# Kernel tuning notes

Measured on AMD Instinct MI355X. Metric: run time of the kernel, lower is better.

The kernel has to match this reference:

```python
import jax, jax.numpy as jnp
import numpy as np

ROPE_BASE = 10000.0

def _rope(x):
    # x: (B, T, H, hd); rotate-half RoPE
    B, T, H, hd = x.shape
    half = hd // 2
    inv_freq = 1.0 / (ROPE_BASE ** (jnp.arange(half, dtype=jnp.float32) / half))
    ang = jnp.arange(T, dtype=jnp.float32)[:, None] * inv_freq[None, :]  # (T, half)
    cos = jnp.cos(ang)[None, :, None, :]
    sin = jnp.sin(ang)[None, :, None, :]
    x1, x2 = x[..., :half], x[..., half:]
    return jnp.concatenate([x1 * cos - x2 * sin, x1 * sin + x2 * cos], axis=-1)

def setup_inputs() -> dict:
    key = jax.random.key(0)
    k1, k2, k3 = jax.random.split(key, 3)
    B, T, D = 4, 2048, 2048
    x = jax.random.normal(k1, (B, T, D), dtype=jnp.float32)
    attn_mask = jnp.ones((B, T), dtype=bool)
    w_qkv = jax.random.normal(k2, (3 * D, D), dtype=jnp.float32) * (D ** -0.5)
    w_out = jax.random.normal(k3, (D, D), dtype=jnp.float32) * (D ** -0.5)
    return {"x": x, "attn_mask": attn_mask, "is_causal": 1, "w_qkv": w_qkv, "w_out": w_out}

def reference(x, attn_mask, is_causal, w_qkv, w_out):
    B, T, D = x.shape
    H = 16
    hd = D // H
    qkv = jnp.einsum('btd,ed->bte', x, w_qkv)  # (B, T, 3D)
    q, k, v = jnp.split(qkv, 3, axis=2)
    q = _rope(q.reshape(B, T, H, hd))
    k = _rope(k.reshape(B, T, H, hd))
    v = v.reshape(B, T, H, hd)
    scale = 1.0 / jnp.sqrt(jnp.float32(hd))
    scores = jnp.einsum('bqhd,bkhd->bhqk', q, k) * scale  # (B, H, T, T)
    if is_causal:
        mask = jnp.tril(jnp.ones((T, T), dtype=bool))[None, None]
    else:
        mask = attn_mask[:, None, None, :]  # (B,1,1,T)
    scores = jnp.where(mask, scores, jnp.finfo(scores.dtype).min)
    attn = jax.nn.softmax(scores, axis=-1)
    y = jnp.einsum('bhqk,bkhd->bqhd', attn, v).reshape(B, T, D)
    return jnp.einsum('btd,ed->bte', y, w_out)
```

## Files before the change

kernel.cpp:

```cpp
#include <hip/hip_runtime.h>
#include <stdint.h>
#include <stddef.h>

typedef float f32x4 __attribute__((ext_vector_type(4)));
typedef __bf16 bf16x8 __attribute__((ext_vector_type(8)));
typedef short s16x4 __attribute__((ext_vector_type(4)));

#define DEVI static __device__ __forceinline__

DEVI float bf2f(unsigned short u) {
  unsigned int x = ((unsigned int)u) << 16;
  float f;
  __builtin_memcpy(&f, &x, 4);
  return f;
}
DEVI unsigned short f2bf(float f) {
  unsigned int x;
  __builtin_memcpy(&x, &f, 4);
  unsigned int r = (x + 0x7fffu + ((x >> 16) & 1u)) >> 16;
  return (unsigned short)r;
}

DEVI void async16(const void* g, void* l) {
  __builtin_amdgcn_global_load_lds((__attribute__((address_space(1))) void*)g,
                                   (__attribute__((address_space(3))) void*)l,
                                   16, 0, 0);
}

#define BAR_LGKM()                                          \
  do {                                                      \
    asm volatile("s_waitcnt lgkmcnt(0)" ::: "memory");      \
    __builtin_amdgcn_s_barrier();                           \
    __builtin_amdgcn_sched_barrier(0);                      \
  } while (0)

#define BAR_VM(N)                                               \
  do {                                                          \
    asm volatile("s_waitcnt vmcnt(" #N ")" ::: "memory");       \
    __builtin_amdgcn_s_barrier();                               \
    __builtin_amdgcn_sched_barrier(0);                          \
  } while (0)

__global__ __launch_bounds__(256) void cvt_bf16(const float* __restrict__ in,
                                                unsigned short* __restrict__ out, int n) {
  int i = (blockIdx.x * 256 + threadIdx.x) * 4;
  if (i >= n) return;
  float4 v = *(const float4*)(in + i);
  s16x4 o;
  o[0] = (short)f2bf(v.x);
  o[1] = (short)f2bf(v.y);
  o[2] = (short)f2bf(v.z);
  o[3] = (short)f2bf(v.w);
  *(s16x4*)(out + i) = o;
}

__global__ __launch_bounds__(256) void rope_table(float* __restrict__ tab) {
  int idx = blockIdx.x * 256 + threadIdx.x;
  if (idx >= 2048 * 64) return;
  int tt = idx >> 6, j = idx & 63;
  float inv = powf(10000.0f, -(float)j * (1.0f / 64.0f));
  float ang = (float)tt * inv;
  tab[tt * 128 + j] = cosf(ang);
  tab[tt * 128 + 64 + j] = sinf(ang);
}

__global__ __launch_bounds__(256) void rope_apply(unsigned short* __restrict__ Qg,
                                                  unsigned short* __restrict__ Kg,
                                                  const float* __restrict__ tab) {
  const float S2 = 0.0883883476483184f * 1.44269504088896341f;
  int idx = blockIdx.x * 256 + threadIdx.x;
  int j4 = idx & 15;
  int tt = (idx >> 4) & 2047;
  int bh = idx >> 15;
  size_t base = ((size_t)bh * 2048 + tt) * 128;
  f32x4 c4 = *(const f32x4*)(tab + tt * 128 + j4 * 4);
  f32x4 s4 = *(const f32x4*)(tab + tt * 128 + 64 + j4 * 4);
  s16x4 q1 = *(const s16x4*)(Qg + base + j4 * 4);
  s16x4 q2 = *(const s16x4*)(Qg + base + 64 + j4 * 4);
  s16x4 k1 = *(const s16x4*)(Kg + base + j4 * 4);
  s16x4 k2 = *(const s16x4*)(Kg + base + 64 + j4 * 4);
  s16x4 o1, o2, p1, p2;
#pragma unroll
  for (int r = 0; r < 4; ++r) {
    float c = c4[r], s = s4[r];
    float a = bf2f((unsigned short)q1[r]), b2 = bf2f((unsigned short)q2[r]);
    o1[r] = (short)f2bf((a * c - b2 * s) * S2);
    o2[r] = (short)f2bf((a * s + b2 * c) * S2);
    float ka = bf2f((unsigned short)k1[r]), kb = bf2f((unsigned short)k2[r]);
    p1[r] = (short)f2bf(ka * c - kb * s);
    p2[r] = (short)f2bf(ka * s + kb * c);
  }
  *(s16x4*)(Qg + base + j4 * 4) = o1;
  *(s16x4*)(Qg + base + 64 + j4 * 4) = o2;
  *(s16x4*)(Kg + base + j4 * 4) = p1;
  *(s16x4*)(Kg + base + 64 + j4 * 4) = p2;
}

template <int EPI>
__global__ __launch_bounds__(512) void gemm256(const unsigned short* __restrict__ A,
                                               const unsigned short* __restrict__ B,
                                               float* __restrict__ C, int M, int N, int K,
                                               unsigned short* __restrict__ Q,
                                               unsigned short* __restrict__ Kk,
                                               unsigned short* __restrict__ VT) {
  __shared__ __attribute__((aligned(128))) unsigned short Al[2][2][8192];
  __shared__ __attribute__((aligned(128))) unsigned short Bl[2][2][8192];
  const int t = threadIdx.x;
  const int lane = t & 63;
  const int w = t >> 6, wr = w >> 2, wc = w & 3;
  const int g = lane >> 4, lr = lane & 15;

  const int id = blockIdx.y * gridDim.x + blockIdx.x;
  const int nwg = gridDim.x * gridDim.y;
  const int wg = (id & 7) * (nwg >> 3) + (id >> 3);
  const int bm = (wg / gridDim.x) * 256, bn = (wg % gridDim.x) * 256;

  const unsigned short* aptr = A + (size_t)bm * K;
  const unsigned short* bptr = B + (size_t)bn * K;

  const int srow = t >> 3;
  const int sslot = (t & 7) ^ (srow & 7);

#define STG(arr, mat, p, h, kt)                                                   \
  do {                                                                            \
    const unsigned short* _s =                                                    \
        (mat) + (size_t)((h) * 128 + srow) * K + (size_t)(kt) * 64 + sslot * 8;   \
    async16(_s, &arr[p][h][t * 8]);                                               \
    async16(_s + (size_t)64 * K, &arr[p][h][t * 8 + 4096]);                       \
  } while (0)

  const int u0 = ((g ^ (lr & 7)) * 8) + lr * 64;
  const int u1 = (((4 + g) ^ (lr & 7)) * 8) + lr * 64;

#define LDA(p, mh)                                                                \
  _Pragma("unroll") for (int mf = 0; mf < 4; ++mf) {                              \
    af[mf][0] = *(const bf16x8*)&Al[p][wr][(mh) * 4096 + mf * 1024 + u0];         \
    af[mf][1] = *(const bf16x8*)&Al[p][wr][(mh) * 4096 + mf * 1024 + u1];         \
  }
#define LDB(p, nh)                                                                \
  _Pragma("unroll") for (int nf = 0; nf < 2; ++nf) {                              \
    bfr[nf][0] = *(const bf16x8*)&Bl[p][wc >> 1][(wc & 1) * 4096 + (nh) * 2048 +  \
                                                 nf * 1024 + u0];                 \
    bfr[nf][1] = *(const bf16x8*)&Bl[p][wc >> 1][(wc & 1) * 4096 + (nh) * 2048 +  \
                                                 nf * 1024 + u1];                 \
  }
#define MMA(mh, nh)                                                               \
  __builtin_amdgcn_s_setprio(1);                                                  \
  _Pragma("unroll") for (int mf = 0; mf < 4; ++mf)                                \
      _Pragma("unroll") for (int nf = 0; nf < 2; ++nf) {                          \
    acc[(mh) * 4 + mf][(nh) * 2 + nf] = __builtin_amdgcn_mfma_f32_16x16x32_bf16(  \
        af[mf][0], bfr[nf][0], acc[(mh) * 4 + mf][(nh) * 2 + nf], 0, 0, 0);       \
    acc[(mh) * 4 + mf][(nh) * 2 + nf] = __builtin_amdgcn_mfma_f32_16x16x32_bf16(  \
        af[mf][1], bfr[nf][1], acc[(mh) * 4 + mf][(nh) * 2 + nf], 0, 0, 0);       \
  }                                                                               \
  __builtin_amdgcn_s_setprio(0);
#define PH_PRE()                                           \
  do {                                                     \
    __builtin_amdgcn_s_barrier();                          \
    asm volatile("s_waitcnt lgkmcnt(0)" ::: "memory");     \
    __builtin_amdgcn_sched_barrier(0);                     \
  } while (0)
#define PH_POST() __builtin_amdgcn_s_barrier();

  f32x4 acc[8][4] = {};

  STG(Al, aptr, 0, 0, 0);
  STG(Al, aptr, 0, 1, 0);
  STG(Bl, bptr, 0, 0, 0);
  STG(Bl, bptr, 0, 1, 0);
  STG(Bl, bptr, 1, 0, 1);
  STG(Bl, bptr, 1, 1, 1);
  asm volatile("s_waitcnt vmcnt(4)" ::: "memory");
  __builtin_amdgcn_s_barrier();
  __builtin_amdgcn_sched_barrier(0);

  const int NITER = K >> 7;
  for (int i = 0; i < NITER; ++i) {
    const bool G = (i + 1 < NITER);
    const int t1 = 2 * i + 1, t2 = 2 * i + 2, t3 = 2 * i + 3;
    bf16x8 af[4][2], bfr[2][2];

    LDA(0, 0);
    LDB(0, 0);
    STG(Al, aptr, 1, 0, t1);
    STG(Al, aptr, 1, 1, t1);
    PH_PRE();
    MMA(0, 0);
    PH_POST();
    LDA(0, 1);
    PH_PRE();
    MMA(1, 0);
    PH_POST();
    LDB(0, 1);
    PH_PRE();
    MMA(1, 1);
    PH_POST();
    LDA(0, 0);
    if (G) {
      STG(Bl, bptr, 0, 0, t2);
      asm volatile("s_waitcnt vmcnt(2)" ::: "memory");
    } else {
      asm volatile("s_waitcnt vmcnt(0)" ::: "memory");
    }
    PH_PRE();
    MMA(0, 1);
    PH_POST();
    LDA(1, 0);
    LDB(1, 0);
    if (G) STG(Bl, bptr, 0, 1, t2);
    PH_PRE();
    MMA(0, 0);
    PH_POST();
    LDA(1, 1);
    if (G) STG(Al, aptr, 0, 0, t2);
    PH_PRE();
    MMA(1, 0);
    PH_POST();
    LDB(1, 1);
    if (G) STG(Al, aptr, 0, 1, t2);
    PH_PRE();
    MMA(1, 1);
    PH_POST();
    LDA(1, 0);
    if (G) {
      STG(Bl, bptr, 1, 0, t3);
      STG(Bl, bptr, 1, 1, t3);
      asm volatile("s_waitcnt vmcnt(4)" ::: "memory");
    }
    PH_PRE();
    MMA(0, 1);
    PH_POST();
  }
#undef STG
#undef LDA
#undef LDB
#undef MMA
#undef PH_PRE
#undef PH_POST

  if (EPI == 0) {
#pragma unroll
    for (int mp = 0; mp < 8; ++mp) {
      int m0 = bm + wr * 128 + (mp >> 2) * 64 + (mp & 3) * 16 + g * 4;
#pragma unroll
      for (int nfi = 0; nfi < 4; ++nfi) {
        int n = bn + wc * 64 + (nfi >> 1) * 32 + (nfi & 1) * 16 + lr;
#pragma unroll
        for (int r = 0; r < 4; ++r) C[(size_t)(m0 + r) * N + n] = acc[mp][nfi][r];
      }
    }
  } else {
    const int bi = bm >> 11;
    const int tbase = bm & 2047;
#pragma unroll
    for (int nfi = 0; nfi < 4; ++nfi) {
      int e = bn + wc * 64 + (nfi >> 1) * 32 + (nfi & 1) * 16 + lr;
      int region = e >> 11;
      int e2 = e & 2047;
      int h = e2 >> 7, d = e2 & 127;
      int bh = bi * 16 + h;
#pragma unroll
      for (int mp = 0; mp < 8; ++mp) {
        int trow = tbase + wr * 128 + (mp >> 2) * 64 + (mp & 3) * 16 + g * 4;
        if (region == 2) {
          s16x4 pk;
#pragma unroll
          for (int r = 0; r < 4; ++r) pk[r] = (short)f2bf(acc[mp][nfi][r]);
          *(s16x4*)(VT + ((size_t)bh * 128 + d) * 2048 + trow) = pk;
        } else {
          unsigned short* dst = (region == 0) ? Q : Kk;
#pragma unroll
          for (int r = 0; r < 4; ++r)
            dst[((size_t)bh * 2048 + trow + r) * 128 + d] = f2bf(acc[mp][nfi][r]);
        }
      }
    }
  }
}

__global__ __launch_bounds__(256) void flash_attn(const unsigned short* __restrict__ Qg,
                                                  const unsigned short* __restrict__ Kg,
                                                  const unsigned short* __restrict__ VTg,
                                                  unsigned short* __restrict__ Yg,
                                                  const int* __restrict__ iscausal,
                                                  const unsigned char* __restrict__ amask) {
  __shared__ __attribute__((aligned(128))) unsigned short Ks[2][64 * 128];
  __shared__ __attribute__((aligned(128))) unsigned short Vs[2][128 * 64];
  __shared__ __attribute__((aligned(128))) unsigned short Ps[4][16 * 72];

  const int t = threadIdx.x, lane = t & 63, w = t >> 6;
  const int g = lane >> 4, lr = lane & 15;
  const int id = blockIdx.x;
  const int xcd = id & 7, j5 = id >> 3;
  const int bh = xcd * 8 + (j5 >> 5);
  const int qbi = 31 - (j5 & 31);
  const int b = bh >> 4;
  const int qb = qbi * 64;
  const int causal = iscausal[0] != 0;
  const int nt = causal ? (qbi + 1) : 32;

  const unsigned short* qrow = Qg + ((size_t)bh * 2048 + qb + w * 16 + lr) * 128;
  bf16x8 qf[4];
#pragma unroll
  for (int ds = 0; ds < 4; ++ds) qf[ds] = *(const bf16x8*)(qrow + ds * 32 + g * 8);

  const unsigned short* Kbase = Kg + (size_t)bh * 2048 * 128;
  const unsigned short* Vbase = VTg + (size_t)bh * 128 * 2048;

  const int rK = t >> 4, sK = ((t & 15) ^ rK);
  const int rV = t >> 3, sV = ((t & 7) ^ ((t >> 3) & 7));

#define STAGE(KT, P)                                                                    \
  do {                                                                                  \
    const int _kv = (KT) * 64;                                                          \
    _Pragma("unroll") for (int c = 0; c < 4; ++c)                                       \
        async16(Kbase + (size_t)(_kv + c * 16 + rK) * 128 + sK * 8,                     \
                &Ks[P][c * 2048 + t * 8]);                                              \
    _Pragma("unroll") for (int c = 0; c < 4; ++c)                                       \
        async16(Vbase + (size_t)(c * 32 + rV) * 2048 + _kv + sV * 8,                    \
                &Vs[P][c * 2048 + t * 8]);                                              \
  } while (0)

  unsigned int oi[4] = {0x3F803F80u, 0x3F803F80u, 0x3F803F80u, 0x3F803F80u};
  bf16x8 ones;
  __builtin_memcpy(&ones, oi, 16);

  f32x4 acc[8] = {};
  f32x4 accl = {0.f, 0.f, 0.f, 0.f};
  float mrow[4] = {-1e30f, -1e30f, -1e30f, -1e30f};

  STAGE(0, 0);

  for (int kt = 0; kt < nt; ++kt) {
    const int p = kt & 1;
    const int kv0 = kt * 64;
    if (kt + 1 < nt) {
      STAGE(kt + 1, p ^ 1);
      BAR_VM(8);
    } else {
      BAR_VM(0);
    }

    f32x4 s[4] = {};
    __builtin_amdgcn_s_setprio(1);
#pragma unroll
    for (int cf = 0; cf < 4; ++cf)
#pragma unroll
      for (int ds = 0; ds < 4; ++ds) {
        bf16x8 kf = *(const bf16x8*)(&Ks[p][(cf * 16 + lr) * 128 + (((ds * 4 + g) ^ lr) * 8)]);
        s[cf] = __builtin_amdgcn_mfma_f32_16x16x32_bf16(qf[ds], kf, s[cf], 0, 0, 0);
      }
    __builtin_amdgcn_s_setprio(0);

    const int q0 = qb + w * 16 + g * 4;
    if (causal) {
      if (kt == qbi) {
#pragma unroll
        for (int cf = 0; cf < 4; ++cf) {
          int kvg = kv0 + cf * 16 + lr;
#pragma unroll
          for (int r = 0; r < 4; ++r)
            if (kvg > q0 + r) s[cf][r] = -1e30f;
        }
      }
    } else {
#pragma unroll
      for (int cf = 0; cf < 4; ++cf) {
        int kvg = kv0 + cf * 16 + lr;
        if (!amask[(size_t)b * 2048 + kvg]) {
#pragma unroll
          for (int r = 0; r < 4; ++r) s[cf][r] = -1e30f;
        }
      }
    }

    f32x4 lm;
#pragma unroll
    for (int r = 0; r < 4; ++r)
      lm[r] = fmaxf(fmaxf(s[0][r], s[1][r]), fmaxf(s[2][r], s[3][r]));
    bool ok = true;
#pragma unroll
    for (int r = 0; r < 4; ++r) ok = ok && (lm[r] <= mrow[r] + 8.0f);
    if (!__all(ok)) {
      f32x4 mx = lm;
#pragma unroll
      for (int off = 8; off >= 1; off >>= 1)
#pragma unroll
        for (int r = 0; r < 4; ++r) mx[r] = fmaxf(mx[r], __shfl_xor(mx[r], off));
#pragma unroll
      for (int r = 0; r < 4; ++r) {
        float mn = fmaxf(mrow[r], mx[r]);
        float corr = exp2f(mrow[r] - mn);
        mrow[r] = mn;
        accl[r] *= corr;
#pragma unroll
        for (int jf = 0; jf < 8; ++jf) acc[jf][r] *= corr;
      }
    }

#pragma unroll
    for (int cf = 0; cf < 4; ++cf)
#pragma unroll
      for (int r = 0; r < 4; ++r) s[cf][r] = exp2f(s[cf][r] - mrow[r]);

    unsigned short* Pw = &Ps[w][0];
#pragma unroll
    for (int cf = 0; cf < 4; ++cf)
#pragma unroll
      for (int r = 0; r < 4; ++r) Pw[(g * 4 + r) * 72 + cf * 16 + lr] = f2bf(s[cf][r]);
    asm volatile("s_waitcnt lgkmcnt(0)" ::: "memory");
    __builtin_amdgcn_sched_barrier(0);

    bf16x8 pa0 = *(const bf16x8*)(Pw + lr * 72 + g * 8);
    bf16x8 pa1 = *(const bf16x8*)(Pw + lr * 72 + 32 + g * 8);

    accl = __builtin_amdgcn_mfma_f32_16x16x32_bf16(pa0, ones, accl, 0, 0, 0);
    accl = __builtin_amdgcn_mfma_f32_16x16x32_bf16(pa1, ones, accl, 0, 0, 0);

    __builtin_amdgcn_s_setprio(1);
#pragma unroll
    for (int jf = 0; jf < 8; ++jf) {
      bf16x8 v0 = *(const bf16x8*)(&Vs[p][(jf * 16 + lr) * 64 + ((g ^ (lr & 7)) * 8)]);
      bf16x8 v1 = *(const bf16x8*)(&Vs[p][(jf * 16 + lr) * 64 + (((4 + g) ^ (lr & 7)) * 8)]);
      acc[jf] = __builtin_amdgcn_mfma_f32_16x16x32_bf16(pa0, v0, acc[jf], 0, 0, 0);
      acc[jf] = __builtin_amdgcn_mfma_f32_16x16x32_bf16(pa1, v1, acc[jf], 0, 0, 0);
    }
    __builtin_amdgcn_s_setprio(0);

    BAR_LGKM();
  }
#undef STAGE

  const int h = bh & 15;
  float rl[4];
#pragma unroll
  for (int r = 0; r < 4; ++r) rl[r] = __builtin_amdgcn_rcpf(accl[r]);
#pragma unroll
  for (int jf = 0; jf < 8; ++jf)
#pragma unroll
    for (int r = 0; r < 4; ++r) {
      int tt = qb + w * 16 + g * 4 + r;
      Yg[((size_t)b * 2048 + tt) * 2048 + h * 128 + jf * 16 + lr] = f2bf(acc[jf][r] * rl[r]);
    }
}

extern "C" void kernel_launch(void* const* d_in, const int* in_sizes, int n_in, void* d_out,
                              int out_size, void* d_ws, size_t ws_size, hipStream_t stream) {
  const float* x = (const float*)d_in[0];
  const unsigned char* amask = (const unsigned char*)d_in[1];
  const int* iscausal = (const int*)d_in[2];
  const float* wqkv = (const float*)d_in[3];
  const float* wout = (const float*)d_in[4];
  float* out = (float*)d_out;

  const size_t MT = 8192, D = 2048, ND = 6144;
  unsigned short* xb = (unsigned short*)d_ws;
  unsigned short* wqkvb = xb + MT * D;
  unsigned short* woutb = wqkvb + ND * D;
  unsigned short* q = woutb + D * D;
  unsigned short* k = q + MT * D;
  unsigned short* vt = k + MT * D;
  unsigned short* y = vt + MT * D;
  float* tab = (float*)(y + MT * D);
  if (ws_size < (size_t)(100663296) * 2 + 2048 * 128 * 4) return;

  cvt_bf16<<<dim3(16384), dim3(256), 0, stream>>>(x, xb, (int)(MT * D));
  cvt_bf16<<<dim3(12288), dim3(256), 0, stream>>>(wqkv, wqkvb, (int)(ND * D));
  cvt_bf16<<<dim3(4096), dim3(256), 0, stream>>>(wout, woutb, (int)(D * D));
  rope_table<<<dim3(512), dim3(256), 0, stream>>>(tab);
  gemm256<1><<<dim3(24, 32), dim3(512), 0, stream>>>(xb, wqkvb, nullptr, 8192, 6144, 2048, q, k, vt);
  rope_apply<<<dim3(8192), dim3(256), 0, stream>>>(q, k, tab);
  flash_attn<<<dim3(2048), dim3(256), 0, stream>>>(q, k, vt, y, iscausal, amask);
  gemm256<0><<<dim3(8, 32), dim3(512), 0, stream>>>(y, woutb, out, 8192, 2048, 2048, nullptr,
                                                    nullptr, nullptr);
}
```

Before: 500.4 us.

## Double-buffer B fragments and drop explicit lgkmcnt waits in GEMM main loop

Reorders the GEMM inner loop's sub-tile traversal and keeps two B-fragment register sets, so an A reload can reuse a B fragment still held in registers. The explicit lgkmcnt(0) waits and sched_barriers are removed, leaving LDS-read waits to the compiler. This aims to cut LDS read traffic and let LDS loads overlap with MFMA. It costs extra VGPRs, and the compiler may reorder loads across barriers or insert its own waits.

```diff
diff --git a/kernel.cpp b/kernel.cpp
--- a/kernel.cpp
+++ b/kernel.cpp
@@ -132,37 +132,32 @@
   const int u0 = ((g ^ (lr & 7)) * 8) + lr * 64;
   const int u1 = (((4 + g) ^ (lr & 7)) * 8) + lr * 64;
 
-#define LDA(p, mh)                                                                \
+#define LDA_(p, mh)                                                               \
   _Pragma("unroll") for (int mf = 0; mf < 4; ++mf) {                              \
     af[mf][0] = *(const bf16x8*)&Al[p][wr][(mh) * 4096 + mf * 1024 + u0];         \
     af[mf][1] = *(const bf16x8*)&Al[p][wr][(mh) * 4096 + mf * 1024 + u1];         \
   }
-#define LDB(p, nh)                                                                \
+#define LDB_(dst, p, nh)                                                          \
   _Pragma("unroll") for (int nf = 0; nf < 2; ++nf) {                              \
-    bfr[nf][0] = *(const bf16x8*)&Bl[p][wc >> 1][(wc & 1) * 4096 + (nh) * 2048 +  \
+    dst[nf][0] = *(const bf16x8*)&Bl[p][wc >> 1][(wc & 1) * 4096 + (nh) * 2048 +  \
                                                  nf * 1024 + u0];                 \
-    bfr[nf][1] = *(const bf16x8*)&Bl[p][wc >> 1][(wc & 1) * 4096 + (nh) * 2048 +  \
+    dst[nf][1] = *(const bf16x8*)&Bl[p][wc >> 1][(wc & 1) * 4096 + (nh) * 2048 +  \
                                                  nf * 1024 + u1];                 \
   }
-#define MMA(mh, nh)                                                               \
+#define MMA_(bsrc, mh, nh)                                                        \
   __builtin_amdgcn_s_setprio(1);                                                  \
   _Pragma("unroll") for (int mf = 0; mf < 4; ++mf)                                \
       _Pragma("unroll") for (int nf = 0; nf < 2; ++nf) {                          \
     acc[(mh) * 4 + mf][(nh) * 2 + nf] = __builtin_amdgcn_mfma_f32_16x16x32_bf16(  \
-        af[mf][0], bfr[nf][0], acc[(mh) * 4 + mf][(nh) * 2 + nf], 0, 0, 0);       \
+        af[mf][0], bsrc[nf][0], acc[(mh) * 4 + mf][(nh) * 2 + nf], 0, 0, 0);      \
     acc[(mh) * 4 + mf][(nh) * 2 + nf] = __builtin_amdgcn_mfma_f32_16x16x32_bf16(  \
-        af[mf][1], bfr[nf][1], acc[(mh) * 4 + mf][(nh) * 2 + nf], 0, 0, 0);       \
+        af[mf][1], bsrc[nf][1], acc[(mh) * 4 + mf][(nh) * 2 + nf], 0, 0, 0);      \
   }                                                                               \
   __builtin_amdgcn_s_setprio(0);
-#define PH_PRE()                                           \
-  do {                                                     \
-    __builtin_amdgcn_s_barrier();                          \
-    asm volatile("s_waitcnt lgkmcnt(0)" ::: "memory");     \
-    __builtin_amdgcn_sched_barrier(0);                     \
-  } while (0)
-#define PH_POST() __builtin_amdgcn_s_barrier();
+#define BARR() __builtin_amdgcn_s_barrier();
 
   f32x4 acc[8][4] = {};
+  bf16x8 af[4][2], bfrA[2][2], bfrB[2][2];
 
   STG(Al, aptr, 0, 0, 0);
   STG(Al, aptr, 0, 1, 0);
@@ -172,71 +167,66 @@
   STG(Bl, bptr, 1, 1, 1);
   asm volatile("s_waitcnt vmcnt(4)" ::: "memory");
   __builtin_amdgcn_s_barrier();
-  __builtin_amdgcn_sched_barrier(0);
 
   const int NITER = K >> 7;
   for (int i = 0; i < NITER; ++i) {
     const bool G = (i + 1 < NITER);
     const int t1 = 2 * i + 1, t2 = 2 * i + 2, t3 = 2 * i + 3;
-    bf16x8 af[4][2], bfr[2][2];
-
-    LDA(0, 0);
-    LDB(0, 0);
+
+    LDA_(0, 0);
+    LDB_(bfrA, 0, 0);
     STG(Al, aptr, 1, 0, t1);
     STG(Al, aptr, 1, 1, t1);
-    PH_PRE();
-    MMA(0, 0);
-    PH_POST();
-    LDA(0, 1);
-    PH_PRE();
-    MMA(1, 0);
-    PH_POST();
-    LDB(0, 1);
-    PH_PRE();
-    MMA(1, 1);
-    PH_POST();
-    LDA(0, 0);
+    BARR();
+    MMA_(bfrA, 0, 0);
+    BARR();
+    LDB_(bfrB, 0, 1);
+    BARR();
+    MMA_(bfrB, 0, 1);
+    BARR();
+    LDA_(0, 1);
+    BARR();
+    MMA_(bfrB, 1, 1);
+    BARR();
     if (G) {
       STG(Bl, bptr, 0, 0, t2);
       asm volatile("s_waitcnt vmcnt(2)" ::: "memory");
     } else {
       asm volatile("s_waitcnt vmcnt(0)" ::: "memory");
     }
-    PH_PRE();
-    MMA(0, 1);
-    PH_POST();
-    LDA(1, 0);
-    LDB(1, 0);
+    BARR();
+    MMA_(bfrA, 1, 0);
+    BARR();
+    LDA_(1, 0);
+    LDB_(bfrA, 1, 0);
     if (G) STG(Bl, bptr, 0, 1, t2);
-    PH_PRE();
-    MMA(0, 0);
-    PH_POST();
-    LDA(1, 1);
+    BARR();
+    MMA_(bfrA, 0, 0);
+    BARR();
+    LDB_(bfrB, 1, 1);
     if (G) STG(Al, aptr, 0, 0, t2);
-    PH_PRE();
-    MMA(1, 0);
-    PH_POST();
-    LDB(1, 1);
+    BARR();
+    MMA_(bfrB, 0, 1);
+    BARR();
+    LDA_(1, 1);
     if (G) STG(Al, aptr, 0, 1, t2);
-    PH_PRE();
-    MMA(1, 1);
-    PH_POST();
-    LDA(1, 0);
+    BARR();
+    MMA_(bfrB, 1, 1);
+    BARR();
     if (G) {
       STG(Bl, bptr, 1, 0, t3);
       STG(Bl, bptr, 1, 1, t3);
       asm volatile("s_waitcnt vmcnt(4)" ::: "memory");
     }
-    PH_PRE();
-    MMA(0, 1);
-    PH_POST();
+    BARR();
+    MMA_(bfrA, 1, 0);
+    BARR();
   }
 #undef STG
-#undef LDA
-#undef LDB
-#undef MMA
-#undef PH_PRE
-#undef PH_POST
+#undef LDA_
+#undef LDB_
+#undef MMA_
+#undef BARR
 
   if (EPI == 0) {
 #pragma unroll
```

After: 485.0 us. -3.1%, faster.
